# Kernel optimization log

Measured on AMD Instinct MI355X. Metric: run time of the kernel, lower is better.

## Reference

```python
import jax, jax.numpy as jnp
import numpy as np

N = 40000; E = 500000; IN = 128; ED = 16; HID = 64; HEADS = 4; OUT = 256; B = 128
NEG = 0.2  # GATv2 leaky_relu negative slope


def _add_self_loops(edge_index, edge_attr, n):
    # PyG add_self_loops with fill_value='mean': loop attr = mean of incoming edge attrs per node
    dst = edge_index[1]
    s = jax.ops.segment_sum(edge_attr, dst, num_segments=n)
    c = jax.ops.segment_sum(jnp.ones((edge_attr.shape[0],), edge_attr.dtype), dst, num_segments=n)
    loop_attr = s / jnp.maximum(c, 1.0)[:, None]
    loops = jnp.arange(n, dtype=edge_index.dtype)
    ei = jnp.concatenate([edge_index, jnp.stack([loops, loops])], axis=1)
    ea = jnp.concatenate([edge_attr, loop_attr], axis=0)
    return ei, ea


def _seg_softmax(logits, seg, n):
    m = jax.ops.segment_max(logits, seg, num_segments=n)
    m = jnp.where(jnp.isfinite(m), m, 0.0)  # guard empty segments
    e = jnp.exp(logits - m[seg])
    z = jax.ops.segment_sum(e, seg, num_segments=n)
    return e / (z[seg] + 1e-16)


def _gatv2(x, src, dst, ea, Wl, bl, Wr, br, We, att, bias, heads, oc, concat):
    n = x.shape[0]
    xl = (x @ Wl + bl).reshape(n, heads, oc)  # lin_l (source/message transform)
    xr = (x @ Wr + br).reshape(n, heads, oc)  # lin_r (target transform)
    ef = (ea @ We).reshape(-1, heads, oc)     # lin_edge (no bias)
    s = jax.nn.leaky_relu(xl[src] + xr[dst] + ef, NEG)  # [Etot,H,C]
    alpha = _seg_softmax(jnp.einsum('ehc,hc->eh', s, att), dst, n)  # scatter-softmax over dst
    out = jax.ops.segment_sum(xl[src] * alpha[..., None], dst, num_segments=n)  # [N,H,C]
    out = out.reshape(n, heads * oc) if concat else out.mean(axis=1)
    return out + bias


def setup_inputs():
    ks = jax.random.split(jax.random.key(0), 32)
    W = lambda i, shp: jax.random.normal(ks[i], shp, jnp.float32) * 0.05
    z = lambda d: jnp.zeros((d,), jnp.float32)
    H = HEADS * HID
    return dict(
        x=jax.random.normal(ks[0], (N, IN), jnp.float32),
        edge_index=jax.random.randint(ks[1], (2, E), 0, N),
        edge_attr=jax.random.normal(ks[2], (E, ED), jnp.float32),
        batch=jnp.sort(jax.random.randint(ks[3], (N,), 0, B)),
        batch_size=B,
        c1_Wl=W(4, (IN, H)), c1_bl=z(H), c1_Wr=W(5, (IN, H)), c1_br=z(H), c1_We=W(6, (ED, H)), c1_att=W(7, (HEADS, HID)), c1_bias=z(H),
        c2_Wl=W(8, (H, H)), c2_bl=z(H), c2_Wr=W(9, (H, H)), c2_br=z(H), c2_We=W(10, (ED, H)), c2_att=W(11, (HEADS, HID)), c2_bias=z(H),
        c3_Wl=W(12, (H, OUT)), c3_bl=z(OUT), c3_Wr=W(13, (H, OUT)), c3_br=z(OUT), c3_We=W(14, (ED, OUT)), c3_att=W(15, (1, OUT)), c3_bias=z(OUT),
        gate_W1=W(16, (OUT, 128)), gate_b1=z(128), gate_W2=W(17, (128, 1)), gate_b2=z(1),
        reg_W1=W(18, (OUT, 128)), reg_b1=z(128), reg_W2=W(19, (128, 2)), reg_b2=z(2),
    )


def reference(x, edge_index, edge_attr, batch, batch_size,
              c1_Wl, c1_bl, c1_Wr, c1_br, c1_We, c1_att, c1_bias,
              c2_Wl, c2_bl, c2_Wr, c2_br, c2_We, c2_att, c2_bias,
              c3_Wl, c3_bl, c3_Wr, c3_br, c3_We, c3_att, c3_bias,
              gate_W1, gate_b1, gate_W2, gate_b2,
              reg_W1, reg_b1, reg_W2, reg_b2):
    # task_type='homo_lumo' path; dropout disabled (inference)
    ei, ea = _add_self_loops(edge_index, edge_attr, N)
    src, dst = ei[0], ei[1]
    h = jax.nn.relu(_gatv2(x, src, dst, ea, c1_Wl, c1_bl, c1_Wr, c1_br, c1_We, c1_att, c1_bias, HEADS, HID, True))
    h = jax.nn.relu(_gatv2(h, src, dst, ea, c2_Wl, c2_bl, c2_Wr, c2_br, c2_We, c2_att, c2_bias, HEADS, HID, True))
    h = _gatv2(h, src, dst, ea, c3_Wl, c3_bl, c3_Wr, c3_br, c3_We, c3_att, c3_bias, 1, OUT, True)
    # AttentionalAggregation pooling
    gate = jax.nn.relu(h @ gate_W1 + gate_b1) @ gate_W2 + gate_b2  # [N,1]
    a = _seg_softmax(gate[:, 0], batch, batch_size)
    g = jax.ops.segment_sum(h * a[:, None], batch, num_segments=batch_size)  # [B,OUT]
    return jax.nn.relu(g @ reg_W1 + reg_b1) @ reg_W2 + reg_b2  # [B,2]
```

## Files before the change

kernel.cpp:

```cpp
#include <hip/hip_runtime.h>
#include <math.h>

constexpr int N_NODES = 40000;
constexpr int N_EDGES = 500000;
constexpr int ETOT    = N_EDGES + N_NODES;
constexpr int IN_DIM  = 128;
constexpr int ED_DIM  = 16;
constexpr int FEAT    = 256;
constexpr int BATCH   = 128;
constexpr float NEG   = 0.2f;
constexpr int NCHUNK  = (N_NODES + 255) / 256;

__global__ __launch_bounds__(256) void k_deg(const int* __restrict__ dst, int* __restrict__ deg)
{
    int e = blockIdx.x * 256 + threadIdx.x;
    if (e >= ETOT) return;
    int v = e < N_EDGES ? dst[e] : e - N_EDGES;
    atomicAdd(&deg[v], 1);
}

__global__ __launch_bounds__(256) void k_scan1(const int* __restrict__ deg, int* __restrict__ bsum)
{
    __shared__ int s[256];
    int t = threadIdx.x;
    int idx = blockIdx.x * 256 + t;
    s[t] = idx < N_NODES ? deg[idx] : 0;
    __syncthreads();
    for (int st = 128; st; st >>= 1) { if (t < st) s[t] += s[t + st]; __syncthreads(); }
    if (t == 0) bsum[blockIdx.x] = s[0];
}

__global__ __launch_bounds__(256) void k_scan2(const int* __restrict__ bsum,
    int* __restrict__ boff, int* __restrict__ rowptr)
{
    __shared__ int s[256];
    int t = threadIdx.x;
    int v = t < NCHUNK ? bsum[t] : 0;
    s[t] = v;
    __syncthreads();
    for (int off = 1; off < 256; off <<= 1) {
        int x = (t >= off) ? s[t - off] : 0;
        __syncthreads();
        s[t] += x;
        __syncthreads();
    }
    if (t < NCHUNK) boff[t] = s[t] - v;
    if (t == 0) rowptr[N_NODES] = ETOT;
}

__global__ __launch_bounds__(256) void k_scan3(const int* __restrict__ deg,
    const int* __restrict__ boff, int* __restrict__ rowptr)
{
    __shared__ int s[256];
    int t = threadIdx.x;
    int idx = blockIdx.x * 256 + t;
    int v = idx < N_NODES ? deg[idx] : 0;
    s[t] = v;
    __syncthreads();
    for (int off = 1; off < 256; off <<= 1) {
        int x = (t >= off) ? s[t - off] : 0;
        __syncthreads();
        s[t] += x;
        __syncthreads();
    }
    if (idx < N_NODES) rowptr[idx] = boff[blockIdx.x] + s[t] - v;
}

__global__ __launch_bounds__(256) void k_fill(const int* __restrict__ srcA, const int* __restrict__ dst,
    const int* __restrict__ rowptr, int* __restrict__ fill, int2* __restrict__ elist2)
{
    int e = blockIdx.x * 256 + threadIdx.x;
    if (e >= ETOT) return;
    int v = e < N_EDGES ? dst[e]  : e - N_EDGES;
    int s = e < N_EDGES ? srcA[e] : e - N_EDGES;
    int pos = rowptr[v] + atomicAdd(&fill[v], 1);
    elist2[pos] = make_int2(s, e);
}

__global__ __launch_bounds__(256) void k_loop_csr(const int2* __restrict__ elist2,
    const int* __restrict__ rowptr, const float* __restrict__ ea, float* __restrict__ loop_attr)
{
    int t = blockIdx.x * 256 + threadIdx.x;
    if (t >= N_NODES * ED_DIM) return;
    int n = t >> 4, d = t & 15;
    int p0 = rowptr[n], p1 = rowptr[n + 1];
    float s = 0.f; int c = 0;
    for (int p = p0; p < p1; ++p) {
        int e = elist2[p].y;
        if (e < N_EDGES) { s += ea[(size_t)e * ED_DIM + d]; ++c; }
    }
    loop_attr[t] = s / (float)(c > 0 ? c : 1);
}

__global__ __launch_bounds__(256) void k_gemm(const float* __restrict__ A, const float* __restrict__ W,
    const float* __restrict__ bias, float* __restrict__ C, int M, int N, int K, int act)
{
    __shared__ float As[16][136];
    __shared__ float Bs[16][136];
    int t = threadIdx.x;
    int bm = blockIdx.x * 128, bn = blockIdx.y * 128;
    int tr = t >> 4, tc = t & 15;
    int mr0 = tr * 8, nc0 = tc * 4;

    int ar0 = t >> 1, ak0 = (t & 1) << 3;
    int bk0 = t >> 5, bn0 = (t & 31) << 2;

    float acc[8][8] = {};

    int r0 = bm + ar0; r0 = r0 < M ? r0 : M - 1;
    float4 avA = *(const float4*)(A + (size_t)r0 * K + ak0);
    float4 avB = *(const float4*)(A + (size_t)r0 * K + ak0 + 4);
    float4 bvA = *(const float4*)(W + (size_t)bk0 * N + bn + bn0);
    float4 bvB = *(const float4*)(W + (size_t)(bk0 + 8) * N + bn + bn0);

    for (int k0 = 0; k0 < K; k0 += 16) {
        __syncthreads();
        As[ak0 + 0][ar0] = avA.x; As[ak0 + 1][ar0] = avA.y;
        As[ak0 + 2][ar0] = avA.z; As[ak0 + 3][ar0] = avA.w;
        As[ak0 + 4][ar0] = avB.x; As[ak0 + 5][ar0] = avB.y;
        As[ak0 + 6][ar0] = avB.z; As[ak0 + 7][ar0] = avB.w;
        *(float4*)&Bs[bk0][bn0]     = bvA;
        *(float4*)&Bs[bk0 + 8][bn0] = bvB;
        __syncthreads();
        if (k0 + 16 < K) {
            avA = *(const float4*)(A + (size_t)r0 * K + k0 + 16 + ak0);
            avB = *(const float4*)(A + (size_t)r0 * K + k0 + 16 + ak0 + 4);
            bvA = *(const float4*)(W + (size_t)(k0 + 16 + bk0) * N + bn + bn0);
            bvB = *(const float4*)(W + (size_t)(k0 + 24 + bk0) * N + bn + bn0);
        }
        #pragma unroll
        for (int k = 0; k < 16; ++k) {
            float4 a0 = *(const float4*)&As[k][mr0];
            float4 a1 = *(const float4*)&As[k][mr0 + 4];
            float4 b0 = *(const float4*)&Bs[k][nc0];
            float4 b1 = *(const float4*)&Bs[k][64 + nc0];
            float am[8] = {a0.x, a0.y, a0.z, a0.w, a1.x, a1.y, a1.z, a1.w};
            float bv[8] = {b0.x, b0.y, b0.z, b0.w, b1.x, b1.y, b1.z, b1.w};
            #pragma unroll
            for (int i = 0; i < 8; ++i)
                #pragma unroll
                for (int j = 0; j < 8; ++j)
                    acc[i][j] = fmaf(am[i], bv[j], acc[i][j]);
        }
    }

    float bb[8];
    #pragma unroll
    for (int j = 0; j < 4; ++j) { bb[j] = bias[bn + nc0 + j]; bb[j + 4] = bias[bn + 64 + nc0 + j]; }
    #pragma unroll
    for (int i = 0; i < 8; ++i) {
        int row = bm + mr0 + i;
        if (row >= M) break;
        float4 o0, o1;
        o0.x = acc[i][0] + bb[0]; o0.y = acc[i][1] + bb[1];
        o0.z = acc[i][2] + bb[2]; o0.w = acc[i][3] + bb[3];
        o1.x = acc[i][4] + bb[4]; o1.y = acc[i][5] + bb[5];
        o1.z = acc[i][6] + bb[6]; o1.w = acc[i][7] + bb[7];
        if (act) {
            o0.x = fmaxf(o0.x, 0.f); o0.y = fmaxf(o0.y, 0.f); o0.z = fmaxf(o0.z, 0.f); o0.w = fmaxf(o0.w, 0.f);
            o1.x = fmaxf(o1.x, 0.f); o1.y = fmaxf(o1.y, 0.f); o1.z = fmaxf(o1.z, 0.f); o1.w = fmaxf(o1.w, 0.f);
        }
        *(float4*)(C + (size_t)row * N + bn + nc0)      = o0;
        *(float4*)(C + (size_t)row * N + bn + 64 + nc0) = o1;
    }
}

static void launch_gemm(const float* A, const float* W, const float* bias, float* C,
                        int M, int N, int K, int act, hipStream_t stream)
{
    dim3 grid((M + 127) / 128, N / 128);
    k_gemm<<<grid, 256, 0, stream>>>(A, W, bias, C, M, N, K, act);
}


#define XELOAD(s) do {                                                                \
    int src_ = __builtin_amdgcn_readfirstlane(eS[s].x);                               \
    int e_   = __builtin_amdgcn_readfirstlane(eS[s].y);                               \
    const float4* eb4_ = reinterpret_cast<const float4*>(                             \
        (e_ < N_EDGES) ? ea + (size_t)e_ * ED_DIM                                     \
                       : loop_attr + (size_t)src_ * ED_DIM);                          \
    evS[s][0] = eb4_[0]; evS[s][1] = eb4_[1];                                         \
    evS[s][2] = eb4_[2]; evS[s][3] = eb4_[3];                                         \
    xlvS[s] = *(const float4*)(xl + (size_t)src_ * FEAT + base);                      \
} while (0)

#define COMPUTE(s) do {                                                               \
    float ef0_ = 0.f, ef1_ = 0.f, ef2_ = 0.f, ef3_ = 0.f;                             \
    const float* ed_ = (const float*)evS[s];                                          \
    _Pragma("unroll")                                                                 \
    for (int d_ = 0; d_ < ED_DIM; ++d_) {                                             \
        float a_ = ed_[d_];                                                           \
        ef0_ = fmaf(a_, weR[d_].x, ef0_); ef1_ = fmaf(a_, weR[d_].y, ef1_);           \
        ef2_ = fmaf(a_, weR[d_].z, ef2_); ef3_ = fmaf(a_, weR[d_].w, ef3_);           \
    }                                                                                 \
    float s0_ = xlvS[s].x + xrv.x + ef0_;                                             \
    float s1_ = xlvS[s].y + xrv.y + ef1_;                                             \
    float s2_ = xlvS[s].z + xrv.z + ef2_;                                             \
    float s3_ = xlvS[s].w + xrv.w + ef3_;                                             \
    s0_ = fmaxf(s0_, 0.f) + NEG * fminf(s0_, 0.f);                                    \
    s1_ = fmaxf(s1_, 0.f) + NEG * fminf(s1_, 0.f);                                    \
    s2_ = fmaxf(s2_, 0.f) + NEG * fminf(s2_, 0.f);                                    \
    s3_ = fmaxf(s3_, 0.f) + NEG * fminf(s3_, 0.f);                                    \
    float l_ = fmaf(s0_, attR.x, fmaf(s1_, attR.y, fmaf(s2_, attR.z, s3_ * attR.w))); \
    l_ += __shfl_xor(l_, 1, 64);                                                      \
    l_ += __shfl_xor(l_, 2, 64);                                                      \
    l_ += __shfl_xor(l_, 4, 64);                                                      \
    l_ += __shfl_xor(l_, 8, 64);                                                      \
    if (H == 1) { l_ += __shfl_xor(l_, 16, 64); l_ += __shfl_xor(l_, 32, 64); }       \
    float nm_ = fmaxf(m, l_);                                                         \
    float sc_ = __expf(m - nm_);                                                      \
    float w_  = __expf(l_ - nm_);                                                     \
    z = fmaf(z, sc_, w_);                                                             \
    m = nm_;                                                                          \
    acc.x = fmaf(acc.x, sc_, w_ * xlvS[s].x);                                         \
    acc.y = fmaf(acc.y, sc_, w_ * xlvS[s].y);                                         \
    acc.z = fmaf(acc.z, sc_, w_ * xlvS[s].z);                                         \
    acc.w = fmaf(acc.w, sc_, w_ * xlvS[s].w);                                         \
} while (0)

template <int H, int RELU>
__global__ __launch_bounds__(256, 4) void k_gat(
    const float* __restrict__ xl, const float* __restrict__ xr,
    const float* __restrict__ ea, const float* __restrict__ loop_attr,
    const int2* __restrict__ elist2, const int* __restrict__ rowptr,
    const float* __restrict__ We, const float* __restrict__ att,
    const float* __restrict__ bias, float* __restrict__ out)
{
    int t = threadIdx.x;
    int lane = t & 63;
    int n = __builtin_amdgcn_readfirstlane(blockIdx.x * 4 + (t >> 6));
    int base = lane * 4;

    float4 weR[ED_DIM];
    #pragma unroll
    for (int d = 0; d < ED_DIM; ++d)
        weR[d] = *(const float4*)(We + d * FEAT + base);

    float4 attR = *(const float4*)(att + base);
    float4 xrv  = *(const float4*)(xr + (size_t)n * FEAT + base);

    float m = -INFINITY, z = 0.f;
    float4 acc = {0.f, 0.f, 0.f, 0.f};

    int p0 = rowptr[n], p1 = rowptr[n + 1];
    int pe = p1 - 1;

    int2   eS[2];
    float4 evS[2][4];
    float4 xlvS[2];

    eS[0] = elist2[p0];
    { int pc = p0 + 1 > pe ? pe : p0 + 1; eS[1] = elist2[pc]; }
    XELOAD(0);

    int p = p0;
    while (true) {
        XELOAD(1);
        { int pn = p + 2 > pe ? pe : p + 2; eS[0] = elist2[pn]; }
        COMPUTE(0);
        if (++p >= p1) break;
        XELOAD(0);
        { int pn = p + 2 > pe ? pe : p + 2; eS[1] = elist2[pn]; }
        COMPUTE(1);
        if (++p >= p1) break;
    }

    float inv = 1.0f / (z + 1e-16f);
    float4 bs = *(const float4*)(bias + base);
    float4 o;
    o.x = fmaf(acc.x, inv, bs.x);
    o.y = fmaf(acc.y, inv, bs.y);
    o.z = fmaf(acc.z, inv, bs.z);
    o.w = fmaf(acc.w, inv, bs.w);
    if (RELU) {
        o.x = fmaxf(o.x, 0.f); o.y = fmaxf(o.y, 0.f);
        o.z = fmaxf(o.z, 0.f); o.w = fmaxf(o.w, 0.f);
    }
    *(float4*)(out + (size_t)n * FEAT + base) = o;
}

__global__ __launch_bounds__(256) void k_gate_score(const float* __restrict__ ghid,
    const float* __restrict__ W2, const float* __restrict__ b2, float* __restrict__ gate)
{
    int lane = threadIdx.x & 63;
    int n = blockIdx.x * 4 + (threadIdx.x >> 6);
    float v = ghid[(size_t)n * 128 + lane] * W2[lane] + ghid[(size_t)n * 128 + lane + 64] * W2[lane + 64];
    #pragma unroll
    for (int off = 32; off > 0; off >>= 1) v += __shfl_xor(v, off, 64);
    if (lane == 0) gate[n] = v + b2[0];
}

__device__ __forceinline__ int lbound(const int* a, int n, int v)
{
    int lo = 0, hi = n;
    while (lo < hi) { int mid = (lo + hi) >> 1; if (a[mid] < v) lo = mid + 1; else hi = mid; }
    return lo;
}

__global__ __launch_bounds__(256) void k_pool(const float* __restrict__ gate,
    const float* __restrict__ h, const int* __restrict__ batch, float* __restrict__ g)
{
    int b = blockIdx.x;
    int t = threadIdx.x;
    __shared__ float red[256];
    int start = lbound(batch, N_NODES, b);
    int end   = lbound(batch, N_NODES, b + 1);

    float mx = -INFINITY;
    for (int n = start + t; n < end; n += 256) mx = fmaxf(mx, gate[n]);
    red[t] = mx; __syncthreads();
    for (int s = 128; s; s >>= 1) { if (t < s) red[t] = fmaxf(red[t], red[t + s]); __syncthreads(); }
    float m = red[0];
    __syncthreads();

    float zs = 0.f;
    for (int n = start + t; n < end; n += 256) zs += __expf(gate[n] - m);
    red[t] = zs; __syncthreads();
    for (int s = 128; s; s >>= 1) { if (t < s) red[t] += red[t + s]; __syncthreads(); }
    float z = red[0];

    float gs = 0.f;
    for (int n = start; n < end; ++n) gs += __expf(gate[n] - m) * h[(size_t)n * FEAT + t];
    g[b * FEAT + t] = gs / (z + 1e-16f);
}

__global__ __launch_bounds__(128) void k_reg(const float* __restrict__ g,
    const float* __restrict__ W1, const float* __restrict__ b1,
    const float* __restrict__ W2, const float* __restrict__ b2, float* __restrict__ out)
{
    int b = blockIdx.x, t = threadIdx.x;
    __shared__ float sg[FEAT];
    sg[t] = g[b * FEAT + t];
    sg[t + 128] = g[b * FEAT + t + 128];
    __syncthreads();
    float hv = b1[t];
    for (int k = 0; k < FEAT; ++k) hv += sg[k] * W1[k * 128 + t];
    hv = fmaxf(hv, 0.f);
    __shared__ float p0s[128], p1s[128];
    p0s[t] = hv * W2[t * 2 + 0];
    p1s[t] = hv * W2[t * 2 + 1];
    __syncthreads();
    for (int s = 64; s; s >>= 1) {
        if (t < s) { p0s[t] += p0s[t + s]; p1s[t] += p1s[t + s]; }
        __syncthreads();
    }
    if (t == 0) { out[b * 2 + 0] = p0s[0] + b2[0]; out[b * 2 + 1] = p1s[0] + b2[1]; }
}

extern "C" void kernel_launch(void* const* d_in, const int* in_sizes, int n_in,
                              void* d_out, int out_size, void* d_ws, size_t ws_size,
                              hipStream_t stream)
{
    const float* x       = (const float*)d_in[0];
    const int*   ei      = (const int*)d_in[1];
    const float* ea      = (const float*)d_in[2];
    const int*   batch   = (const int*)d_in[3];
    const float* c1_Wl   = (const float*)d_in[5];
    const float* c1_bl   = (const float*)d_in[6];
    const float* c1_Wr   = (const float*)d_in[7];
    const float* c1_br   = (const float*)d_in[8];
    const float* c1_We   = (const float*)d_in[9];
    const float* c1_att  = (const float*)d_in[10];
    const float* c1_bias = (const float*)d_in[11];
    const float* c2_Wl   = (const float*)d_in[12];
    const float* c2_bl   = (const float*)d_in[13];
    const float* c2_Wr   = (const float*)d_in[14];
    const float* c2_br   = (const float*)d_in[15];
    const float* c2_We   = (const float*)d_in[16];
    const float* c2_att  = (const float*)d_in[17];
    const float* c2_bias = (const float*)d_in[18];
    const float* c3_Wl   = (const float*)d_in[19];
    const float* c3_bl   = (const float*)d_in[20];
    const float* c3_Wr   = (const float*)d_in[21];
    const float* c3_br   = (const float*)d_in[22];
    const float* c3_We   = (const float*)d_in[23];
    const float* c3_att  = (const float*)d_in[24];
    const float* c3_bias = (const float*)d_in[25];
    const float* gate_W1 = (const float*)d_in[26];
    const float* gate_b1 = (const float*)d_in[27];
    const float* gate_W2 = (const float*)d_in[28];
    const float* gate_b2 = (const float*)d_in[29];
    const float* reg_W1  = (const float*)d_in[30];
    const float* reg_b1  = (const float*)d_in[31];
    const float* reg_W2  = (const float*)d_in[32];
    const float* reg_b2  = (const float*)d_in[33];

    const int* srcArr = ei;
    const int* dstArr = ei + N_EDGES;

    float* ws = (float*)d_ws;
    size_t off = 0;
    auto alloc = [&](size_t nf) { float* p = ws + off; off += (nf + 63) & ~(size_t)63; return p; };
    float* xl        = alloc((size_t)N_NODES * FEAT);
    float* xr        = alloc((size_t)N_NODES * FEAT);
    float* h         = alloc((size_t)N_NODES * FEAT);
    float* loop_attr = alloc((size_t)N_NODES * ED_DIM);
    float* gpool     = alloc((size_t)BATCH * FEAT);
    int* ibase  = (int*)(ws + off);
    int* deg    = ibase;
    int* fill   = ibase + N_NODES;
    int* rowptr = ibase + 2 * N_NODES;
    int* bsum   = ibase + 3 * N_NODES + 64;
    int* boff   = bsum + 256;
    int2* elist2 = (int2*)(boff + 256);

    float* ghid = xl;
    float* gate = xr;

    hipMemsetAsync(deg, 0, (size_t)2 * N_NODES * sizeof(int), stream);

    k_deg<<<(ETOT + 255) / 256, 256, 0, stream>>>(dstArr, deg);
    k_scan1<<<NCHUNK, 256, 0, stream>>>(deg, bsum);
    k_scan2<<<1, 256, 0, stream>>>(bsum, boff, rowptr);
    k_scan3<<<NCHUNK, 256, 0, stream>>>(deg, boff, rowptr);
    k_fill<<<(ETOT + 255) / 256, 256, 0, stream>>>(srcArr, dstArr, rowptr, fill, elist2);
    k_loop_csr<<<(N_NODES * ED_DIM + 255) / 256, 256, 0, stream>>>(elist2, rowptr, ea, loop_attr);

    launch_gemm(x, c1_Wl, c1_bl, xl, N_NODES, FEAT, IN_DIM, 0, stream);
    launch_gemm(x, c1_Wr, c1_br, xr, N_NODES, FEAT, IN_DIM, 0, stream);
    k_gat<4, 1><<<N_NODES / 4, 256, 0, stream>>>(xl, xr, ea, loop_attr, elist2, rowptr,
                                                 c1_We, c1_att, c1_bias, h);
    launch_gemm(h, c2_Wl, c2_bl, xl, N_NODES, FEAT, FEAT, 0, stream);
    launch_gemm(h, c2_Wr, c2_br, xr, N_NODES, FEAT, FEAT, 0, stream);
    k_gat<4, 1><<<N_NODES / 4, 256, 0, stream>>>(xl, xr, ea, loop_attr, elist2, rowptr,
                                                 c2_We, c2_att, c2_bias, h);
    launch_gemm(h, c3_Wl, c3_bl, xl, N_NODES, FEAT, FEAT, 0, stream);
    launch_gemm(h, c3_Wr, c3_br, xr, N_NODES, FEAT, FEAT, 0, stream);
    k_gat<1, 0><<<N_NODES / 4, 256, 0, stream>>>(xl, xr, ea, loop_attr, elist2, rowptr,
                                                 c3_We, c3_att, c3_bias, h);

    launch_gemm(h, gate_W1, gate_b1, ghid, N_NODES, 128, FEAT, 1, stream);
    k_gate_score<<<N_NODES / 4, 256, 0, stream>>>(ghid, gate_W2, gate_b2, gate);
    k_pool<<<BATCH, 256, 0, stream>>>(gate, h, batch, gpool);
    k_reg<<<BATCH, 128, 0, stream>>>(gpool, reg_W1, reg_b1, reg_W2, reg_b2, (float*)d_out);
}
```

Before: 1.211 ms.

## Replace FP32 SIMT GEMM with split-bf16 MFMA GEMM (3-term emulation)

```diff
diff --git a/kernel.cpp b/kernel.cpp
--- a/kernel.cpp
+++ b/kernel.cpp
@@ -11,6 +11,9 @@
 constexpr float NEG   = 0.2f;
 constexpr int NCHUNK  = (N_NODES + 255) / 256;
 
+typedef __bf16 bf16x8 __attribute__((ext_vector_type(8)));
+typedef float  f32x4  __attribute__((ext_vector_type(4)));
+
 __global__ __launch_bounds__(256) void k_deg(const int* __restrict__ dst, int* __restrict__ deg)
 {
     int e = blockIdx.x * 256 + threadIdx.x;
@@ -92,86 +95,138 @@
     loop_attr[t] = s / (float)(c > 0 ? c : 1);
 }
 
-__global__ __launch_bounds__(256) void k_gemm(const float* __restrict__ A, const float* __restrict__ W,
-    const float* __restrict__ bias, float* __restrict__ C, int M, int N, int K, int act)
-{
-    __shared__ float As[16][136];
-    __shared__ float Bs[16][136];
+__device__ __forceinline__ void bsplit(float x, unsigned short& h, unsigned short& l)
+{
+    unsigned u = __float_as_uint(x);
+    unsigned r = (u + 0x7FFFu + ((u >> 16) & 1u)) >> 16;
+    h = (unsigned short)r;
+    float rem = x - __uint_as_float(r << 16);
+    unsigned u2 = __float_as_uint(rem);
+    l = (unsigned short)((u2 + 0x7FFFu + ((u2 >> 16) & 1u)) >> 16);
+}
+
+__global__ __launch_bounds__(256) void k_cvt(const float* __restrict__ X,
+    unsigned short* __restrict__ Xh, unsigned short* __restrict__ Xl, int n4)
+{
+    int i = blockIdx.x * 256 + threadIdx.x;
+    if (i >= n4) return;
+    float4 v = ((const float4*)X)[i];
+    ushort4 h, l;
+    bsplit(v.x, h.x, l.x);
+    bsplit(v.y, h.y, l.y);
+    bsplit(v.z, h.z, l.z);
+    bsplit(v.w, h.w, l.w);
+    ((ushort4*)Xh)[i] = h;
+    ((ushort4*)Xl)[i] = l;
+}
+
+__global__ __launch_bounds__(256) void k_cvtT(const float* __restrict__ W,
+    unsigned short* __restrict__ WhT, unsigned short* __restrict__ WlT, int K, int N)
+{
+    int i = blockIdx.x * 256 + threadIdx.x;
+    if (i >= K * N) return;
+    int k = i / N, n = i - k * N;
+    unsigned short h, l;
+    bsplit(W[i], h, l);
+    WhT[(size_t)n * K + k] = h;
+    WlT[(size_t)n * K + k] = l;
+}
+
+__global__ __launch_bounds__(256) void k_mgemm(
+    const unsigned short* __restrict__ Ah, const unsigned short* __restrict__ Al,
+    const unsigned short* __restrict__ BhT, const unsigned short* __restrict__ BlT,
+    const float* __restrict__ bias, float* __restrict__ C,
+    int M, int N, int K, int act)
+{
+    __shared__ uint4 sAh[512], sAl[512], sBh[512], sBl[512];
+
     int t = threadIdx.x;
     int bm = blockIdx.x * 128, bn = blockIdx.y * 128;
-    int tr = t >> 4, tc = t & 15;
-    int mr0 = tr * 8, nc0 = tc * 4;
-
-    int ar0 = t >> 1, ak0 = (t & 1) << 3;
-    int bk0 = t >> 5, bn0 = (t & 31) << 2;
-
-    float acc[8][8] = {};
-
-    int r0 = bm + ar0; r0 = r0 < M ? r0 : M - 1;
-    float4 avA = *(const float4*)(A + (size_t)r0 * K + ak0);
-    float4 avB = *(const float4*)(A + (size_t)r0 * K + ak0 + 4);
-    float4 bvA = *(const float4*)(W + (size_t)bk0 * N + bn + bn0);
-    float4 bvB = *(const float4*)(W + (size_t)(bk0 + 8) * N + bn + bn0);
-
-    for (int k0 = 0; k0 < K; k0 += 16) {
-        __syncthreads();
-        As[ak0 + 0][ar0] = avA.x; As[ak0 + 1][ar0] = avA.y;
-        As[ak0 + 2][ar0] = avA.z; As[ak0 + 3][ar0] = avA.w;
-        As[ak0 + 4][ar0] = avB.x; As[ak0 + 5][ar0] = avB.y;
-        As[ak0 + 6][ar0] = avB.z; As[ak0 + 7][ar0] = avB.w;
-        *(float4*)&Bs[bk0][bn0]     = bvA;
-        *(float4*)&Bs[bk0 + 8][bn0] = bvB;
-        __syncthreads();
-        if (k0 + 16 < K) {
-            avA = *(const float4*)(A + (size_t)r0 * K + k0 + 16 + ak0);
-            avB = *(const float4*)(A + (size_t)r0 * K + k0 + 16 + ak0 + 4);
-            bvA = *(const float4*)(W + (size_t)(k0 + 16 + bk0) * N + bn + bn0);
-            bvB = *(const float4*)(W + (size_t)(k0 + 24 + bk0) * N + bn + bn0);
+    int lane = t & 63;
+    int w = t >> 6;
+    int mh = w >> 1, nh = w & 1;
+
+    int sT = t >> 6, sq = (t >> 4) & 3, slm = t & 15;
+    int am0 = bm + sT * 16 + slm;        am0 = am0 < M ? am0 : M - 1;
+    int am1 = bm + (sT + 4) * 16 + slm;  am1 = am1 < M ? am1 : M - 1;
+    int bn0 = bn + sT * 16 + slm;
+    int bn1 = bn + (sT + 4) * 16 + slm;
+    size_t aoff0 = (size_t)am0 * K + sq * 8;
+    size_t aoff1 = (size_t)am1 * K + sq * 8;
+    size_t boff0 = (size_t)bn0 * K + sq * 8;
+    size_t boff1 = (size_t)bn1 * K + sq * 8;
+
+    f32x4 acc[4][4] = {};
+
+    uint4 rAh0 = *(const uint4*)(Ah + aoff0),  rAh1 = *(const uint4*)(Ah + aoff1);
+    uint4 rAl0 = *(const uint4*)(Al + aoff0),  rAl1 = *(const uint4*)(Al + aoff1);
+    uint4 rBh0 = *(const uint4*)(BhT + boff0), rBh1 = *(const uint4*)(BhT + boff1);
+    uint4 rBl0 = *(const uint4*)(BlT + boff0), rBl1 = *(const uint4*)(BlT + boff1);
+
+    int nk = K >> 5;
+    for (int ks = 0; ks < nk; ++ks) {
+        sAh[t] = rAh0; sAh[t + 256] = rAh1;
+        sAl[t] = rAl0; sAl[t + 256] = rAl1;
+        sBh[t] = rBh0; sBh[t + 256] = rBh1;
+        sBl[t] = rBl0; sBl[t + 256] = rBl1;
+        __syncthreads();
+        if (ks + 1 < nk) {
+            int k8 = (ks + 1) << 5;
+            rAh0 = *(const uint4*)(Ah + aoff0 + k8);  rAh1 = *(const uint4*)(Ah + aoff1 + k8);
+            rAl0 = *(const uint4*)(Al + aoff0 + k8);  rAl1 = *(const uint4*)(Al + aoff1 + k8);
+            rBh0 = *(const uint4*)(BhT + boff0 + k8); rBh1 = *(const uint4*)(BhT + boff1 + k8);
+            rBl0 = *(const uint4*)(BlT + boff0 + k8); rBl1 = *(const uint4*)(BlT + boff1 + k8);
+        }
+        bf16x8 fah[4], fal[4], fbh[4], fbl[4];
+        #pragma unroll
+        for (int mt = 0; mt < 4; ++mt) {
+            fah[mt] = __builtin_bit_cast(bf16x8, sAh[(mh * 4 + mt) * 64 + lane]);
+            fal[mt] = __builtin_bit_cast(bf16x8, sAl[(mh * 4 + mt) * 64 + lane]);
         }
         #pragma unroll
-        for (int k = 0; k < 16; ++k) {
-            float4 a0 = *(const float4*)&As[k][mr0];
-            float4 a1 = *(const float4*)&As[k][mr0 + 4];
-            float4 b0 = *(const float4*)&Bs[k][nc0];
-            float4 b1 = *(const float4*)&Bs[k][64 + nc0];
-            float am[8] = {a0.x, a0.y, a0.z, a0.w, a1.x, a1.y, a1.z, a1.w};
-            float bv[8] = {b0.x, b0.y, b0.z, b0.w, b1.x, b1.y, b1.z, b1.w};
+        for (int nt = 0; nt < 4; ++nt) {
+            fbh[nt] = __builtin_bit_cast(bf16x8, sBh[(nh * 4 + nt) * 64 + lane]);
+            fbl[nt] = __builtin_bit_cast(bf16x8, sBl[(nh * 4 + nt) * 64 + lane]);
+        }
+        #pragma unroll
+        for (int mt = 0; mt < 4; ++mt)
             #pragma unroll
-            for (int i = 0; i < 8; ++i)
-                #pragma unroll
-                for (int j = 0; j < 8; ++j)
-                    acc[i][j] = fmaf(am[i], bv[j], acc[i][j]);
+            for (int nt = 0; nt < 4; ++nt) {
+                acc[mt][nt] = __builtin_amdgcn_mfma_f32_16x16x32_bf16(fah[mt], fbh[nt], acc[mt][nt], 0, 0, 0);
+                acc[mt][nt] = __builtin_amdgcn_mfma_f32_16x16x32_bf16(fah[mt], fbl[nt], acc[mt][nt], 0, 0, 0);
+                acc[mt][nt] = __builtin_amdgcn_mfma_f32_16x16x32_bf16(fal[mt], fbh[nt], acc[mt][nt], 0, 0, 0);
+            }
+        __syncthreads();
+    }
+
+    int q = lane >> 4, lm = lane & 15;
+    #pragma unroll
+    for (int nt = 0; nt < 4; ++nt) {
+        int col = bn + nh * 64 + nt * 16 + lm;
+        float bb = bias[col];
+        #pragma unroll
+        for (int mt = 0; mt < 4; ++mt) {
+            #pragma unroll
+            for (int i = 0; i < 4; ++i) {
+                int row = bm + mh * 64 + mt * 16 + q * 4 + i;
+                if (row < M) {
+                    float o = acc[mt][nt][i] + bb;
+                    if (act) o = fmaxf(o, 0.f);
+                    C[(size_t)row * N + col] = o;
+                }
+            }
         }
     }
-
-    float bb[8];
-    #pragma unroll
-    for (int j = 0; j < 4; ++j) { bb[j] = bias[bn + nc0 + j]; bb[j + 4] = bias[bn + 64 + nc0 + j]; }
-    #pragma unroll
-    for (int i = 0; i < 8; ++i) {
-        int row = bm + mr0 + i;
-        if (row >= M) break;
-        float4 o0, o1;
-        o0.x = acc[i][0] + bb[0]; o0.y = acc[i][1] + bb[1];
-        o0.z = acc[i][2] + bb[2]; o0.w = acc[i][3] + bb[3];
-        o1.x = acc[i][4] + bb[4]; o1.y = acc[i][5] + bb[5];
-        o1.z = acc[i][6] + bb[6]; o1.w = acc[i][7] + bb[7];
-        if (act) {
-            o0.x = fmaxf(o0.x, 0.f); o0.y = fmaxf(o0.y, 0.f); o0.z = fmaxf(o0.z, 0.f); o0.w = fmaxf(o0.w, 0.f);
-            o1.x = fmaxf(o1.x, 0.f); o1.y = fmaxf(o1.y, 0.f); o1.z = fmaxf(o1.z, 0.f); o1.w = fmaxf(o1.w, 0.f);
-        }
-        *(float4*)(C + (size_t)row * N + bn + nc0)      = o0;
-        *(float4*)(C + (size_t)row * N + bn + 64 + nc0) = o1;
-    }
-}
-
-static void launch_gemm(const float* A, const float* W, const float* bias, float* C,
-                        int M, int N, int K, int act, hipStream_t stream)
+}
+
+static void launch_mgemm(const unsigned short* Ah, const unsigned short* Al,
+                         const unsigned short* BhT, const unsigned short* BlT,
+                         const float* bias, float* C, int M, int N, int K, int act,
+                         hipStream_t stream)
 {
     dim3 grid((M + 127) / 128, N / 128);
-    k_gemm<<<grid, 256, 0, stream>>>(A, W, bias, C, M, N, K, act);
-}
-
+    k_mgemm<<<grid, 256, 0, stream>>>(Ah, Al, BhT, BlT, bias, C, M, N, K, act);
+}
 
 #define XELOAD(s) do {                                                                \
     int src_ = __builtin_amdgcn_readfirstlane(eS[s].x);                               \
@@ -396,6 +451,12 @@
     float* h         = alloc((size_t)N_NODES * FEAT);
     float* loop_attr = alloc((size_t)N_NODES * ED_DIM);
     float* gpool     = alloc((size_t)BATCH * FEAT);
+    unsigned short* Ah = (unsigned short*)alloc((size_t)N_NODES * FEAT / 2);
+    unsigned short* Al = (unsigned short*)alloc((size_t)N_NODES * FEAT / 2);
+    unsigned short* wlT_h = (unsigned short*)alloc(FEAT * FEAT / 2);
+    unsigned short* wlT_l = (unsigned short*)alloc(FEAT * FEAT / 2);
+    unsigned short* wrT_h = (unsigned short*)alloc(FEAT * FEAT / 2);
+    unsigned short* wrT_l = (unsigned short*)alloc(FEAT * FEAT / 2);
     int* ibase  = (int*)(ws + off);
     int* deg    = ibase;
     int* fill   = ibase + N_NODES;
@@ -416,20 +477,43 @@
     k_fill<<<(ETOT + 255) / 256, 256, 0, stream>>>(srcArr, dstArr, rowptr, fill, elist2);
     k_loop_csr<<<(N_NODES * ED_DIM + 255) / 256, 256, 0, stream>>>(elist2, rowptr, ea, loop_attr);
 
-    launch_gemm(x, c1_Wl, c1_bl, xl, N_NODES, FEAT, IN_DIM, 0, stream);
-    launch_gemm(x, c1_Wr, c1_br, xr, N_NODES, FEAT, IN_DIM, 0, stream);
+    {
+        int n4 = N_NODES * IN_DIM / 4;
+        k_cvt<<<(n4 + 255) / 256, 256, 0, stream>>>(x, Ah, Al, n4);
+        k_cvtT<<<(IN_DIM * FEAT + 255) / 256, 256, 0, stream>>>(c1_Wl, wlT_h, wlT_l, IN_DIM, FEAT);
+        k_cvtT<<<(IN_DIM * FEAT + 255) / 256, 256, 0, stream>>>(c1_Wr, wrT_h, wrT_l, IN_DIM, FEAT);
+        launch_mgemm(Ah, Al, wlT_h, wlT_l, c1_bl, xl, N_NODES, FEAT, IN_DIM, 0, stream);
+        launch_mgemm(Ah, Al, wrT_h, wrT_l, c1_br, xr, N_NODES, FEAT, IN_DIM, 0, stream);
+    }
     k_gat<4, 1><<<N_NODES / 4, 256, 0, stream>>>(xl, xr, ea, loop_attr, elist2, rowptr,
                                                  c1_We, c1_att, c1_bias, h);
-    launch_gemm(h, c2_Wl, c2_bl, xl, N_NODES, FEAT, FEAT, 0, stream);
-    launch_gemm(h, c2_Wr, c2_br, xr, N_NODES, FEAT, FEAT, 0, stream);
+    {
+        int n4 = N_NODES * FEAT / 4;
+        k_cvt<<<(n4 + 255) / 256, 256, 0, stream>>>(h, Ah, Al, n4);
+        k_cvtT<<<(FEAT * FEAT + 255) / 256, 256, 0, stream>>>(c2_Wl, wlT_h, wlT_l, FEAT, FEAT);
+        k_cvtT<<<(FEAT * FEAT + 255) / 256, 256, 0, stream>>>(c2_Wr, wrT_h, wrT_l, FEAT, FEAT);
+        launch_mgemm(Ah, Al, wlT_h, wlT_l, c2_bl, xl, N_NODES, FEAT, FEAT, 0, stream);
+        launch_mgemm(Ah, Al, wrT_h, wrT_l, c2_br, xr, N_NODES, FEAT, FEAT, 0, stream);
+    }
     k_gat<4, 1><<<N_NODES / 4, 256, 0, stream>>>(xl, xr, ea, loop_attr, elist2, rowptr,
                                                  c2_We, c2_att, c2_bias, h);
-    launch_gemm(h, c3_Wl, c3_bl, xl, N_NODES, FEAT, FEAT, 0, stream);
-    launch_gemm(h, c3_Wr, c3_br, xr, N_NODES, FEAT, FEAT, 0, stream);
+    {
+        int n4 = N_NODES * FEAT / 4;
+        k_cvt<<<(n4 + 255) / 256, 256, 0, stream>>>(h, Ah, Al, n4);
+        k_cvtT<<<(FEAT * FEAT + 255) / 256, 256, 0, stream>>>(c3_Wl, wlT_h, wlT_l, FEAT, FEAT);
+        k_cvtT<<<(FEAT * FEAT + 255) / 256, 256, 0, stream>>>(c3_Wr, wrT_h, wrT_l, FEAT, FEAT);
+        launch_mgemm(Ah, Al, wlT_h, wlT_l, c3_bl, xl, N_NODES, FEAT, FEAT, 0, stream);
+        launch_mgemm(Ah, Al, wrT_h, wrT_l, c3_br, xr, N_NODES, FEAT, FEAT, 0, stream);
+    }
     k_gat<1, 0><<<N_NODES / 4, 256, 0, stream>>>(xl, xr, ea, loop_attr, elist2, rowptr,
                                                  c3_We, c3_att, c3_bias, h);
 
-    launch_gemm(h, gate_W1, gate_b1, ghid, N_NODES, 128, FEAT, 1, stream);
+    {
+        int n4 = N_NODES * FEAT / 4;
+        k_cvt<<<(n4 + 255) / 256, 256, 0, stream>>>(h, Ah, Al, n4);
+        k_cvtT<<<(FEAT * 128 + 255) / 256, 256, 0, stream>>>(gate_W1, wlT_h, wlT_l, FEAT, 128);
+        launch_mgemm(Ah, Al, wlT_h, wlT_l, gate_b1, ghid, N_NODES, 128, FEAT, 1, stream);
+    }
     k_gate_score<<<N_NODES / 4, 256, 0, stream>>>(ghid, gate_W2, gate_b2, gate);
     k_pool<<<BATCH, 256, 0, stream>>>(gate, h, batch, gpool);
     k_reg<<<BATCH, 128, 0, stream>>>(gpool, reg_W1, reg_b1, reg_W2, reg_b2, (float*)d_out);
```

New measurement: 1.122 ms. 7.4% less time.
